# Kernel optimization log

Measured on AMD Instinct MI355X. Metric: run time of the kernel, lower is better.

The kernel has to match this reference:

```python
import math
import jax, jax.numpy as jnp
import numpy as np

B, H, W, C = 4, 64, 64, 96
SSM_RATIO = 2.0
D_INNER = int(SSM_RATIO * C)   # 192
D_STATE = 4
DT_RANK = math.ceil(C / 16)    # 6
K = 4                          # 4 scan directions
D_CONV = 3


def layer_norm(x, g, b, eps=1e-5):
    mu = jnp.mean(x, axis=-1, keepdims=True)
    var = jnp.var(x, axis=-1, keepdims=True)
    return (x - mu) / jnp.sqrt(var + eps) * g + b


def cross_scan(x):
    # x: (B, D, H, W) -> (B, K=4, D, L); dirs: row-major, col-major, and their reverses
    b, d, h, w = x.shape
    s0 = x.reshape(b, d, h * w)
    s1 = jnp.transpose(x, (0, 1, 3, 2)).reshape(b, d, h * w)
    return jnp.stack([s0, s1, s0[..., ::-1], s1[..., ::-1]], axis=1)


def cross_merge(ys, h, w):
    # ys: (B, K=4, D, L) -> (B, D, L); inverse of cross_scan, summed over directions
    b, k, d, L = ys.shape
    ys = ys[:, 0:2] + ys[:, 2:4][..., ::-1]
    y0 = ys[:, 0]
    y1 = jnp.transpose(ys[:, 1].reshape(b, d, w, h), (0, 1, 3, 2)).reshape(b, d, L)
    return y0 + y1


def selective_scan(u, dt, A, Bm, Cm, D4):
    # u, dt: (B,K,D,L); A: (K,D,N); Bm, Cm: (B,K,N,L); D4: (K,D)
    u_l = jnp.moveaxis(u, -1, 0)    # (L,B,K,D)
    dt_l = jnp.moveaxis(dt, -1, 0)
    B_l = jnp.moveaxis(Bm, -1, 0)   # (L,B,K,N)
    C_l = jnp.moveaxis(Cm, -1, 0)

    def step(h, inp):
        u_t, dt_t, B_t, C_t = inp
        dA = jnp.exp(dt_t[..., None] * A)                              # (B,K,D,N)
        h = h * dA + dt_t[..., None] * B_t[:, :, None, :] * u_t[..., None]
        y = jnp.sum(h * C_t[:, :, None, :], axis=-1)                   # (B,K,D)
        return h, y

    h0 = jnp.zeros(u.shape[:3] + (A.shape[-1],), u.dtype)
    _, ys = jax.lax.scan(step, h0, (u_l, dt_l, B_l, C_l))
    return jnp.moveaxis(ys, 0, -1) + D4[None, :, :, None] * u


def _block(x_rgb, x_e, in_proj_x_w, in_proj_e_w, conv_x_w, conv_x_b, conv_e_w, conv_e_b,
           x_proj_weight, dt_projs_weight, dt_projs_bias, A_logs, Ds,
           ln_r_g, ln_r_b, ln_e_g, ln_e_b, out_proj_x_w, out_proj_e_w):
    b, h, w, c = x_rgb.shape
    Din, N, R = D_INNER, D_STATE, DT_RANK

    xr = jnp.einsum('bhwc,dc->bhwd', x_rgb, in_proj_x_w)
    xe = jnp.einsum('bhwc,dc->bhwd', x_e, in_proj_e_w)
    xr = jnp.transpose(xr, (0, 3, 1, 2))  # (B,Din,H,W)
    xe = jnp.transpose(xe, (0, 3, 1, 2))

    def dwconv(x, wt, bias):
        y = jax.lax.conv_general_dilated(x, wt, (1, 1), 'SAME', feature_group_count=Din)
        return jax.nn.silu(y + bias[None, :, None, None])

    xr = dwconv(xr, conv_x_w, conv_x_b)
    xe = dwconv(xe, conv_e_w, conv_e_b)

    xs_r = cross_scan(xr)  # (B,K,Din,L)
    xs_e = cross_scan(xe)

    def proj(xs):
        dbl = jnp.einsum('bkdl,kcd->bkcl', xs, x_proj_weight)
        dtl, Bm, Cm = dbl[:, :, :R], dbl[:, :, R:R + N], dbl[:, :, R + N:]
        dtl = jnp.einsum('bkrl,kdr->bkdl', dtl, dt_projs_weight)
        dtl = jax.nn.softplus(dtl + dt_projs_bias[None, :, :, None])
        return dtl, Bm, Cm

    dt_r, B_r, C_r = proj(xs_r)
    dt_e, B_e, C_e = proj(xs_e)

    A = -jnp.exp(A_logs).reshape(K, Din, N)
    D4 = Ds.reshape(K, Din)

    # cross fusion: each modality's scan reads out through the OTHER modality's C
    y_r = selective_scan(xs_r, dt_r, A, B_r, C_e, D4)
    y_e = selective_scan(xs_e, dt_e, A, B_e, C_r, D4)

    y_r = cross_merge(y_r, h, w)  # (B,Din,L)
    y_e = cross_merge(y_e, h, w)

    y_r = layer_norm(jnp.transpose(y_r, (0, 2, 1)), ln_r_g, ln_r_b).reshape(b, h, w, Din)
    y_e = layer_norm(jnp.transpose(y_e, (0, 2, 1)), ln_e_g, ln_e_b).reshape(b, h, w, Din)

    out_r = jnp.einsum('bhwd,cd->bhwc', y_r, out_proj_x_w)
    out_e = jnp.einsum('bhwd,cd->bhwc', y_e, out_proj_e_w)

    # residual add of the wrapping block (drop_path=0, mlp_ratio=0)
    return x_rgb + out_r, x_e + out_e


def setup_inputs():
    key = jax.random.key(0)
    ks = jax.random.split(key, 16)
    N, R, Din = D_STATE, DT_RANK, D_INNER

    def rn(k, shape, s=0.02):
        return (jax.random.normal(k, shape) * s).astype(jnp.float32)

    # dt bias: inverse-softplus of dt ~ U[1e-3, 0.1]  (mamba-style init)
    dt = jnp.exp(jax.random.uniform(ks[10], (K, Din)) * (np.log(0.1) - np.log(1e-3)) + np.log(1e-3))
    dt_bias = dt + jnp.log(-jnp.expm1(-dt))

    return {
        'x_rgb': jax.random.normal(ks[0], (B, H, W, C), jnp.float32),
        'x_e': jax.random.normal(ks[1], (B, H, W, C), jnp.float32),
        'in_proj_x_w': rn(ks[2], (Din, C)),
        'in_proj_e_w': rn(ks[3], (Din, C)),
        'conv_x_w': rn(ks[4], (Din, 1, D_CONV, D_CONV), 0.1),
        'conv_x_b': jnp.zeros((Din,), jnp.float32),
        'conv_e_w': rn(ks[5], (Din, 1, D_CONV, D_CONV), 0.1),
        'conv_e_b': jnp.zeros((Din,), jnp.float32),
        'x_proj_weight': rn(ks[6], (K, R + 2 * N, Din)),
        'dt_projs_weight': rn(ks[7], (K, Din, R), R ** -0.5),
        'dt_projs_bias': dt_bias.astype(jnp.float32),
        'A_logs': jnp.log(jnp.tile(jnp.arange(1, N + 1, dtype=jnp.float32), (K * Din, 1))),
        'Ds': jnp.ones((K * Din,), jnp.float32),
        'ln_r_g': jnp.ones((Din,), jnp.float32),
        'ln_r_b': jnp.zeros((Din,), jnp.float32),
        'ln_e_g': jnp.ones((Din,), jnp.float32),
        'ln_e_b': jnp.zeros((Din,), jnp.float32),
        'out_proj_x_w': rn(ks[8], (C, Din)),
        'out_proj_e_w': rn(ks[9], (C, Din)),
    }


def reference(x_rgb, x_e, in_proj_x_w, in_proj_e_w, conv_x_w, conv_x_b, conv_e_w, conv_e_b,
              x_proj_weight, dt_projs_weight, dt_projs_bias, A_logs, Ds,
              ln_r_g, ln_r_b, ln_e_g, ln_e_b, out_proj_x_w, out_proj_e_w):
    return _block(x_rgb, x_e, in_proj_x_w, in_proj_e_w, conv_x_w, conv_x_b, conv_e_w, conv_e_b,
                  x_proj_weight, dt_projs_weight, dt_projs_bias, A_logs, Ds,
                  ln_r_g, ln_r_b, ln_e_g, ln_e_b, out_proj_x_w, out_proj_e_w)
```

## Files before the change

kernel.cpp:

```cpp
#include <hip/hip_runtime.h>

#define BB 4
#define HH 64
#define WW 64
#define CC 96
#define DIN 192
#define NS 4
#define RR 6
#define KK 4
#define LL 4096
#define NPOS (BB*LL)
#define NPD ((size_t)NPOS*DIN)
#define NDBC ((size_t)BB*KK*LL*14)
#define NCHUNK 128
#define CLEN 32
#define NCHAIN 32
#define PB 8

__device__ __forceinline__ int map_pos(int k, int l){
  switch(k){
    case 0: return l;
    case 1: { int wi=l>>6, hi=l&63; return hi*WW+wi; }
    case 2: return LL-1-l;
    default:{ int lr=LL-1-l; int wi=lr>>6, hi=lr&63; return hi*WW+wi; }
  }
}
__device__ __forceinline__ int pos_stride(int k){
  return (k==0) ? 1 : (k==1) ? WW : (k==2) ? -1 : -WW;
}

__global__ __launch_bounds__(DIN) void inproj_kernel(
    const float* __restrict__ x_rgb, const float* __restrict__ x_e,
    const float* __restrict__ w_r,   const float* __restrict__ w_e,
    float* __restrict__ xproj_r,    float* __restrict__ xproj_e){
  int blk = blockIdx.x;
  int m = blk / (NPOS/PB); int g = blk % (NPOS/PB);
  size_t rem0 = (size_t)g * PB;
  const float* x = m ? x_e : x_rgb;
  const float* w = m ? w_e : w_r;
  float* o = m ? xproj_e : xproj_r;
  __shared__ float xs[PB][CC];
  __shared__ float wt[DIN][17];
  int t = threadIdx.x;
  for(int idx=t; idx<PB*CC; idx+=DIN) xs[idx/CC][idx%CC] = x[rem0*CC + idx];
  float acc[PB];
  #pragma unroll
  for(int p=0;p<PB;p++) acc[p]=0.f;
  for(int c0=0; c0<CC; c0+=16){
    __syncthreads();
    for(int idx=t; idx<DIN*16; idx+=DIN){
      int dd = idx>>4, cc = idx&15;
      wt[dd][cc] = w[(size_t)dd*CC + c0 + cc];
    }
    __syncthreads();
    #pragma unroll
    for(int cc=0; cc<16; cc++){
      float wv = wt[t][cc];
      #pragma unroll
      for(int p=0;p<PB;p++) acc[p] += xs[p][c0+cc]*wv;
    }
  }
  #pragma unroll
  for(int p=0;p<PB;p++) o[(rem0+p)*DIN + t] = acc[p];
}

__global__ __launch_bounds__(DIN) void conv_kernel(
    const float* __restrict__ xproj_r, const float* __restrict__ xproj_e,
    const float* __restrict__ cw_r, const float* __restrict__ cb_r,
    const float* __restrict__ cw_e, const float* __restrict__ cb_e,
    float* __restrict__ xconv_r, float* __restrict__ xconv_e){
  int blk = blockIdx.x;
  int m = blk / NPOS; int rem = blk % NPOS;
  int b = rem / LL, p = rem % LL;
  int y = p >> 6, x = p & 63;
  const float* in = (m ? xproj_e : xproj_r) + (size_t)b*LL*DIN;
  const float* cw = m ? cw_e : cw_r;
  const float* cb = m ? cb_e : cb_r;
  float* out = m ? xconv_e : xconv_r;
  int d = threadIdx.x;
  float acc = cb[d];
  #pragma unroll
  for(int dy=-1;dy<=1;dy++){
    int yy = y+dy; if(yy<0 || yy>=HH) continue;
    #pragma unroll
    for(int dx=-1;dx<=1;dx++){
      int xx = x+dx; if(xx<0 || xx>=WW) continue;
      acc += in[(size_t)(yy*WW+xx)*DIN + d] * cw[d*9 + (dy+1)*3 + (dx+1)];
    }
  }
  float s = acc / (1.f + __expf(-acc));
  out[(size_t)(b*LL+p)*DIN + d] = s;
}

#define TPOS 32
__global__ __launch_bounds__(256) void projbc_kernel(
    const float* __restrict__ xconv_r, const float* __restrict__ xconv_e,
    const float* __restrict__ xpw,
    float* __restrict__ dtBC_r, float* __restrict__ dtBC_e){
  int blk = blockIdx.x;
  int m = blk / (BB*LL/TPOS); int rem = blk % (BB*LL/TPOS);
  int b = rem / (LL/TPOS); int p0 = (rem % (LL/TPOS)) * TPOS;
  const float* xc = (m ? xconv_e : xconv_r) + ((size_t)b*LL + p0)*DIN;
  float* o = (m ? dtBC_e : dtBC_r) + (size_t)b*KK*LL*14;

  __shared__ float xs[TPOS*97];
  __shared__ float wsd[56*97];

  int t = threadIdx.x;
  int g = t >> 5;
  int pl = t & 31;

  float acc[7];
  #pragma unroll
  for(int j=0;j<7;j++) acc[j]=0.f;

  for(int dt0=0; dt0<DIN; dt0+=96){
    __syncthreads();
    for(int idx=t; idx<TPOS*96; idx+=256){
      int r = idx/96, ccol = idx%96;
      xs[r*97+ccol] = xc[(size_t)r*DIN + dt0 + ccol];
    }
    for(int idx=t; idx<56*96; idx+=256){
      int r = idx/96, ccol = idx%96;
      wsd[r*97+ccol] = xpw[(size_t)r*DIN + dt0 + ccol];
    }
    __syncthreads();
    const float* xrow = &xs[pl*97];
    #pragma unroll 4
    for(int d=0; d<96; d++){
      float xv = xrow[d];
      #pragma unroll
      for(int j=0;j<7;j++) acc[j] += wsd[(g*7+j)*97 + d]*xv;
    }
  }

  int p = p0 + pl;
  int ptr_ = (p&63)*64 + (p>>6);
  #pragma unroll
  for(int j=0;j<7;j++){
    int cbar = g*7+j;
    int k = cbar/14, c = cbar%14;
    int l = (k==0) ? p : (k==1) ? ptr_ : (k==2) ? (LL-1-p) : (LL-1-ptr_);
    o[((size_t)k*LL + l)*14 + c] = acc[j];
  }
}

__global__ __launch_bounds__(DIN) void scan_p1_kernel(
    const float* __restrict__ xconv_r, const float* __restrict__ xconv_e,
    const float* __restrict__ dtBC_r, const float* __restrict__ dtBC_e,
    const float* __restrict__ dtw, const float* __restrict__ dtb,
    const float* __restrict__ A_logs,
    float* __restrict__ trans_S, float* __restrict__ sumdt){
  int ch = blockIdx.x / NCHUNK;
  int cidx = blockIdx.x % NCHUNK;
  int m = ch >> 4, b = (ch>>2)&3, k = ch&3;
  int d = threadIdx.x;
  int l0 = cidx*CLEN;

  float4 al = *(const float4*)&A_logs[(size_t)(k*DIN+d)*NS];
  float A0=-__expf(al.x), A1=-__expf(al.y), A2=-__expf(al.z), A3=-__expf(al.w);
  float Wd[RR];
  #pragma unroll
  for(int r=0;r<RR;r++) Wd[r] = dtw[((size_t)k*DIN + d)*RR + r];
  float bias = dtb[k*DIN+d];

  const float* xc    = (m ? xconv_e : xconv_r) + (size_t)b*LL*DIN;
  const float* dbc_m = (m ? dtBC_e : dtBC_r) + ((size_t)b*KK + k)*LL*14;

  __shared__ float4 db4[CLEN][4];
  __shared__ float u_s[CLEN*DIN];
  float* dbf = (float*)db4;

  for(int idx=d; idx<CLEN*14; idx+=DIN){
    int i = idx/14, j = idx%14;
    int slot = (j<6) ? (8+j) : (j-6);
    dbf[i*16+slot] = dbc_m[(size_t)l0*14 + idx];
  }
  int stride = pos_stride(k);
  int pos0 = map_pos(k, l0);
  #pragma unroll 8
  for(int i=0;i<CLEN;i++)
    u_s[i*DIN+d] = xc[(size_t)(pos0+i*stride)*DIN + d];
  __syncthreads();

  float h0=0.f,h1=0.f,h2=0.f,h3=0.f,sd=0.f;
  #pragma unroll 4
  for(int i=0;i<CLEN;i++){
    float4 Bv  = db4[i][0];
    float4 d03 = db4[i][2];
    float4 d45 = db4[i][3];
    float dtr = fmaf(d03.x,Wd[0], fmaf(d03.y,Wd[1], fmaf(d03.z,Wd[2],
                fmaf(d03.w,Wd[3], fmaf(d45.x,Wd[4], fmaf(d45.y,Wd[5], bias))))));
    float dt = fmaxf(dtr,0.f) + __logf(1.f + __expf(-fabsf(dtr)));
    sd += dt;
    float u = u_s[i*DIN + d];
    float dtu = dt*u;
    h0 = fmaf(h0, __expf(dt*A0), dtu*Bv.x);
    h1 = fmaf(h1, __expf(dt*A1), dtu*Bv.y);
    h2 = fmaf(h2, __expf(dt*A2), dtu*Bv.z);
    h3 = fmaf(h3, __expf(dt*A3), dtu*Bv.w);
  }
  size_t base = ((size_t)(ch*NCHUNK + cidx)*NS)*DIN + d;
  trans_S[base          ] = h0;
  trans_S[base +   DIN  ] = h1;
  trans_S[base + 2*DIN  ] = h2;
  trans_S[base + 3*DIN  ] = h3;
  sumdt[(size_t)(ch*NCHUNK + cidx)*DIN + d] = sd;
}

__global__ __launch_bounds__(DIN) void scan_p2_kernel(
    const float* __restrict__ trans_S, const float* __restrict__ sumdt,
    const float* __restrict__ A_logs, float* __restrict__ hin){
  int ch = blockIdx.x; int k = ch & 3; int d = threadIdx.x;
  float4 al = *(const float4*)&A_logs[(size_t)(k*DIN+d)*NS];
  float A[NS] = {-__expf(al.x), -__expf(al.y), -__expf(al.z), -__expf(al.w)};
  float h[NS] = {0.f,0.f,0.f,0.f};
  for(int c0=0;c0<NCHUNK;c0+=4){
    float S[4][NS], sdv[4];
    #pragma unroll
    for(int cc=0;cc<4;cc++){
      size_t base = ((size_t)(ch*NCHUNK + c0+cc)*NS)*DIN + d;
      #pragma unroll
      for(int n=0;n<NS;n++) S[cc][n] = trans_S[base + (size_t)n*DIN];
      sdv[cc] = sumdt[(size_t)(ch*NCHUNK + c0+cc)*DIN + d];
    }
    #pragma unroll
    for(int cc=0;cc<4;cc++){
      size_t base = ((size_t)(ch*NCHUNK + c0+cc)*NS)*DIN + d;
      #pragma unroll
      for(int n=0;n<NS;n++) hin[base + (size_t)n*DIN] = h[n];
      #pragma unroll
      for(int n=0;n<NS;n++) h[n] = fmaf(h[n], __expf(A[n]*sdv[cc]), S[cc][n]);
    }
  }
}

__global__ __launch_bounds__(DIN) void scan_p3_kernel(
    const float* __restrict__ xconv_r, const float* __restrict__ xconv_e,
    const float* __restrict__ dtBC_r, const float* __restrict__ dtBC_e,
    const float* __restrict__ dtw, const float* __restrict__ dtb,
    const float* __restrict__ A_logs, const float* __restrict__ Ds,
    const float* __restrict__ hin,
    float* __restrict__ ym_r, float* __restrict__ ym_e){
  int ch = blockIdx.x / NCHUNK;
  int cidx = blockIdx.x % NCHUNK;
  int m = ch >> 4, b = (ch>>2)&3, k = ch&3;
  int d = threadIdx.x;
  int l0 = cidx*CLEN;

  float4 al = *(const float4*)&A_logs[(size_t)(k*DIN+d)*NS];
  float A0=-__expf(al.x), A1=-__expf(al.y), A2=-__expf(al.z), A3=-__expf(al.w);
  float Wd[RR];
  #pragma unroll
  for(int r=0;r<RR;r++) Wd[r] = dtw[((size_t)k*DIN + d)*RR + r];
  float bias = dtb[k*DIN+d];
  float Dv = Ds[k*DIN+d];

  const float* xc    = (m ? xconv_e : xconv_r) + (size_t)b*LL*DIN;
  const float* dbc_m = (m ? dtBC_e : dtBC_r) + ((size_t)b*KK + k)*LL*14;
  const float* dbc_o = (m ? dtBC_r : dtBC_e) + ((size_t)b*KK + k)*LL*14;
  float* ym = (m ? ym_e : ym_r) + (size_t)b*LL*DIN;

  __shared__ float4 db4[CLEN][4];
  __shared__ float u_s[CLEN*DIN];
  float* dbf = (float*)db4;

  for(int idx=d; idx<CLEN*14; idx+=DIN){
    int i = idx/14, j = idx%14;
    int slot = (j<6) ? (8+j) : (j-6);
    dbf[i*16+slot] = dbc_m[(size_t)l0*14 + idx];
  }
  for(int idx=d; idx<CLEN*NS; idx+=DIN){
    int i = idx>>2, j = idx&3;
    dbf[i*16 + 4 + j] = dbc_o[(size_t)(l0+i)*14 + 10 + j];
  }
  int stride = pos_stride(k);
  int pos0 = map_pos(k, l0);
  #pragma unroll 8
  for(int i=0;i<CLEN;i++)
    u_s[i*DIN+d] = xc[(size_t)(pos0+i*stride)*DIN + d];
  __syncthreads();

  size_t hbase = ((size_t)(ch*NCHUNK + cidx)*NS)*DIN + d;
  float h0=hin[hbase], h1=hin[hbase+DIN], h2=hin[hbase+2*DIN], h3=hin[hbase+3*DIN];

  #pragma unroll 4
  for(int i=0;i<CLEN;i++){
    float4 Bv  = db4[i][0];
    float4 Cv  = db4[i][1];
    float4 d03 = db4[i][2];
    float4 d45 = db4[i][3];
    float dtr = fmaf(d03.x,Wd[0], fmaf(d03.y,Wd[1], fmaf(d03.z,Wd[2],
                fmaf(d03.w,Wd[3], fmaf(d45.x,Wd[4], fmaf(d45.y,Wd[5], bias))))));
    float dt = fmaxf(dtr,0.f) + __logf(1.f + __expf(-fabsf(dtr)));
    float u = u_s[i*DIN + d];
    float dtu = dt*u;
    h0 = fmaf(h0, __expf(dt*A0), dtu*Bv.x);
    h1 = fmaf(h1, __expf(dt*A1), dtu*Bv.y);
    h2 = fmaf(h2, __expf(dt*A2), dtu*Bv.z);
    h3 = fmaf(h3, __expf(dt*A3), dtu*Bv.w);
    float y = fmaf(h0,Cv.x, fmaf(h1,Cv.y, fmaf(h2,Cv.z, fmaf(h3,Cv.w, Dv*u))));
    atomicAdd(&ym[(size_t)(pos0+i*stride)*DIN + d], y);
  }
}

__global__ __launch_bounds__(DIN) void ln_out_kernel(
    const float* __restrict__ ym_r, const float* __restrict__ ym_e,
    const float* __restrict__ ln_rg, const float* __restrict__ ln_rb,
    const float* __restrict__ ln_eg, const float* __restrict__ ln_eb,
    const float* __restrict__ opw_r, const float* __restrict__ opw_e,
    const float* __restrict__ x_rgb, const float* __restrict__ x_e,
    float* __restrict__ out){
  int blk = blockIdx.x;
  int m = blk / (NPOS/PB); int g = blk % (NPOS/PB);
  size_t rem0 = (size_t)g * PB;
  const float* ym = (m ? ym_e : ym_r) + rem0*DIN;
  int t = threadIdx.x;
  int wid = t>>6;

  float v[PB];
  #pragma unroll
  for(int p=0;p<PB;p++) v[p] = ym[(size_t)p*DIN + t];

  __shared__ float red_s[PB][3], red_q[PB][3];
  #pragma unroll
  for(int p=0;p<PB;p++){
    float s = v[p], q = v[p]*v[p];
    #pragma unroll
    for(int off=32; off>0; off>>=1){ s += __shfl_down(s,off); q += __shfl_down(q,off); }
    if((t&63)==0){ red_s[p][wid]=s; red_q[p][wid]=q; }
  }
  __syncthreads();

  const float* gg = m ? ln_eg : ln_rg;
  const float* be = m ? ln_eb : ln_rb;
  __shared__ float yn_s[PB][DIN];
  float gv = gg[t], bv = be[t];
  #pragma unroll
  for(int p=0;p<PB;p++){
    float S = red_s[p][0]+red_s[p][1]+red_s[p][2];
    float Q = red_q[p][0]+red_q[p][1]+red_q[p][2];
    float mu  = S*(1.f/DIN);
    float var = Q*(1.f/DIN) - mu*mu;
    float inv = rsqrtf(var + 1e-5f);
    yn_s[p][t] = (v[p]-mu)*inv*gv + bv;
  }
  __syncthreads();

  int c = t % CC;
  int pbase = t / CC;
  const float* w = (m ? opw_e : opw_r) + (size_t)c*DIN;
  float acc[4] = {0.f,0.f,0.f,0.f};
  for(int dd=0; dd<DIN; dd++){
    float wv = w[dd];
    #pragma unroll
    for(int pp=0;pp<4;pp++) acc[pp] += yn_s[pbase + 2*pp][dd]*wv;
  }
  const float* xin = m ? x_e : x_rgb;
  #pragma unroll
  for(int pp=0;pp<4;pp++){
    size_t rem = rem0 + pbase + 2*pp;
    size_t oi = (size_t)m*NPOS*CC + rem*CC + c;
    out[oi] = acc[pp] + xin[rem*CC + c];
  }
}

extern "C" void kernel_launch(void* const* d_in, const int* in_sizes, int n_in,
                              void* d_out, int out_size, void* d_ws, size_t ws_size,
                              hipStream_t stream){
  const float* x_rgb = (const float*)d_in[0];
  const float* x_e   = (const float*)d_in[1];
  const float* ipw_r = (const float*)d_in[2];
  const float* ipw_e = (const float*)d_in[3];
  const float* cw_r  = (const float*)d_in[4];
  const float* cb_r  = (const float*)d_in[5];
  const float* cw_e  = (const float*)d_in[6];
  const float* cb_e  = (const float*)d_in[7];
  const float* xpw   = (const float*)d_in[8];
  const float* dtw   = (const float*)d_in[9];
  const float* dtb   = (const float*)d_in[10];
  const float* Alog  = (const float*)d_in[11];
  const float* Ds_   = (const float*)d_in[12];
  const float* ln_rg = (const float*)d_in[13];
  const float* ln_rb = (const float*)d_in[14];
  const float* ln_eg = (const float*)d_in[15];
  const float* ln_eb = (const float*)d_in[16];
  const float* opw_r = (const float*)d_in[17];
  const float* opw_e = (const float*)d_in[18];
  float* out = (float*)d_out;

  float* ws = (float*)d_ws;
  float* xproj_r = ws;
  float* xproj_e = ws + NPD;
  float* xconv_r = ws + 2*NPD;
  float* xconv_e = ws + 3*NPD;
  float* dtBC_r  = ws + 4*NPD;
  float* dtBC_e  = ws + 4*NPD + NDBC;
  float* trans_S = ws + 4*NPD + 2*NDBC;
  float* sumdt   = trans_S + (size_t)NCHAIN*NCHUNK*NS*DIN;
  float* hin     = sumdt   + (size_t)NCHAIN*NCHUNK*DIN;
  float* ym_r = xproj_r;
  float* ym_e = xproj_e;

  inproj_kernel<<<2*NPOS/PB, DIN, 0, stream>>>(x_rgb, x_e, ipw_r, ipw_e, xproj_r, xproj_e);
  conv_kernel<<<2*NPOS, DIN, 0, stream>>>(xproj_r, xproj_e, cw_r, cb_r, cw_e, cb_e, xconv_r, xconv_e);
  projbc_kernel<<<2*BB*(LL/TPOS), 256, 0, stream>>>(xconv_r, xconv_e, xpw, dtBC_r, dtBC_e);
  scan_p1_kernel<<<NCHAIN*NCHUNK, DIN, 0, stream>>>(xconv_r, xconv_e, dtBC_r, dtBC_e,
                                                    dtw, dtb, Alog, trans_S, sumdt);
  scan_p2_kernel<<<NCHAIN, DIN, 0, stream>>>(trans_S, sumdt, Alog, hin);
  hipMemsetAsync(ym_r, 0, 2*NPD*sizeof(float), stream);
  scan_p3_kernel<<<NCHAIN*NCHUNK, DIN, 0, stream>>>(xconv_r, xconv_e, dtBC_r, dtBC_e,
                                                    dtw, dtb, Alog, Ds_, hin, ym_r, ym_e);
  ln_out_kernel<<<2*NPOS/PB, DIN, 0, stream>>>(ym_r, ym_e, ln_rg, ln_rb, ln_eg, ln_eb,
                                               opw_r, opw_e, x_rgb, x_e, out);
}
```

Before: 463.3 us.

## Pair forward and reverse scan directions per block, drop atomics and memset

Each scan_p3 block now handles a forward direction chunk and the matching chunk of its reversed direction, which touch the same spatial positions. The block loads the shared u tile once, writes the first result with a plain store and read-modify-writes the second. Row and column directions go to two separate output buffers that the LN kernel sums, so the float atomics and the output memset are no longer needed. The cost is two extra full-size workspace buffers, an extra read in the LN kernel, and twice the serial work per block with half as many blocks.

```diff
diff --git a/kernel.cpp b/kernel.cpp
--- a/kernel.cpp
+++ b/kernel.cpp
@@ -241,71 +241,118 @@
     const float* __restrict__ dtw, const float* __restrict__ dtb,
     const float* __restrict__ A_logs, const float* __restrict__ Ds,
     const float* __restrict__ hin,
-    float* __restrict__ ym_r, float* __restrict__ ym_e){
-  int ch = blockIdx.x / NCHUNK;
-  int cidx = blockIdx.x % NCHUNK;
-  int m = ch >> 4, b = (ch>>2)&3, k = ch&3;
+    float* __restrict__ ym_a_r, float* __restrict__ ym_a_e,
+    float* __restrict__ ym_b_r, float* __restrict__ ym_b_e){
+  int blk = blockIdx.x;
+  int cidx = blk % NCHUNK;
+  int rem  = blk / NCHUNK;
+  int pg = rem & 1; rem >>= 1;
+  int b  = rem & 3; int m = rem >> 2;
+  int kA = pg, kB = pg + 2;
+  int cidx2 = NCHUNK-1-cidx;
+  int l0A = cidx*CLEN, l0B = cidx2*CLEN;
+
   int d = threadIdx.x;
-  int l0 = cidx*CLEN;
-
-  float4 al = *(const float4*)&A_logs[(size_t)(k*DIN+d)*NS];
-  float A0=-__expf(al.x), A1=-__expf(al.y), A2=-__expf(al.z), A3=-__expf(al.w);
-  float Wd[RR];
-  #pragma unroll
-  for(int r=0;r<RR;r++) Wd[r] = dtw[((size_t)k*DIN + d)*RR + r];
-  float bias = dtb[k*DIN+d];
-  float Dv = Ds[k*DIN+d];
-
-  const float* xc    = (m ? xconv_e : xconv_r) + (size_t)b*LL*DIN;
-  const float* dbc_m = (m ? dtBC_e : dtBC_r) + ((size_t)b*KK + k)*LL*14;
-  const float* dbc_o = (m ? dtBC_r : dtBC_e) + ((size_t)b*KK + k)*LL*14;
-  float* ym = (m ? ym_e : ym_r) + (size_t)b*LL*DIN;
-
-  __shared__ float4 db4[CLEN][4];
+  int st = pos_stride(kA);
+  int pos0 = map_pos(kA, l0A);
+
+  const float* xc = (m ? xconv_e : xconv_r) + (size_t)b*LL*DIN;
+  const float* dbc_own = (m ? dtBC_e : dtBC_r) + (size_t)b*KK*LL*14;
+  const float* dbc_oth = (m ? dtBC_r : dtBC_e) + (size_t)b*KK*LL*14;
+  float* ym = (pg==0) ? (m ? ym_a_e : ym_a_r) : (m ? ym_b_e : ym_b_r);
+  ym += (size_t)b*LL*DIN;
+
+  __shared__ float4 db4A[CLEN][4];
+  __shared__ float4 db4B[CLEN][4];
   __shared__ float u_s[CLEN*DIN];
-  float* dbf = (float*)db4;
+  float* dbfA = (float*)db4A;
+  float* dbfB = (float*)db4B;
 
   for(int idx=d; idx<CLEN*14; idx+=DIN){
     int i = idx/14, j = idx%14;
     int slot = (j<6) ? (8+j) : (j-6);
-    dbf[i*16+slot] = dbc_m[(size_t)l0*14 + idx];
+    dbfA[i*16+slot] = dbc_own[((size_t)kA*LL + l0A)*14 + idx];
+    dbfB[i*16+slot] = dbc_own[((size_t)kB*LL + l0B)*14 + idx];
   }
   for(int idx=d; idx<CLEN*NS; idx+=DIN){
     int i = idx>>2, j = idx&3;
-    dbf[i*16 + 4 + j] = dbc_o[(size_t)(l0+i)*14 + 10 + j];
-  }
-  int stride = pos_stride(k);
-  int pos0 = map_pos(k, l0);
+    dbfA[i*16 + 4 + j] = dbc_oth[((size_t)kA*LL + l0A + i)*14 + 10 + j];
+    dbfB[i*16 + 4 + j] = dbc_oth[((size_t)kB*LL + l0B + i)*14 + 10 + j];
+  }
   #pragma unroll 8
   for(int i=0;i<CLEN;i++)
-    u_s[i*DIN+d] = xc[(size_t)(pos0+i*stride)*DIN + d];
+    u_s[i*DIN+d] = xc[(size_t)(pos0+i*st)*DIN + d];
   __syncthreads();
 
-  size_t hbase = ((size_t)(ch*NCHUNK + cidx)*NS)*DIN + d;
-  float h0=hin[hbase], h1=hin[hbase+DIN], h2=hin[hbase+2*DIN], h3=hin[hbase+3*DIN];
-
-  #pragma unroll 4
-  for(int i=0;i<CLEN;i++){
-    float4 Bv  = db4[i][0];
-    float4 Cv  = db4[i][1];
-    float4 d03 = db4[i][2];
-    float4 d45 = db4[i][3];
-    float dtr = fmaf(d03.x,Wd[0], fmaf(d03.y,Wd[1], fmaf(d03.z,Wd[2],
-                fmaf(d03.w,Wd[3], fmaf(d45.x,Wd[4], fmaf(d45.y,Wd[5], bias))))));
-    float dt = fmaxf(dtr,0.f) + __logf(1.f + __expf(-fabsf(dtr)));
-    float u = u_s[i*DIN + d];
-    float dtu = dt*u;
-    h0 = fmaf(h0, __expf(dt*A0), dtu*Bv.x);
-    h1 = fmaf(h1, __expf(dt*A1), dtu*Bv.y);
-    h2 = fmaf(h2, __expf(dt*A2), dtu*Bv.z);
-    h3 = fmaf(h3, __expf(dt*A3), dtu*Bv.w);
-    float y = fmaf(h0,Cv.x, fmaf(h1,Cv.y, fmaf(h2,Cv.z, fmaf(h3,Cv.w, Dv*u))));
-    atomicAdd(&ym[(size_t)(pos0+i*stride)*DIN + d], y);
+  {
+    int k = kA;
+    float4 al = *(const float4*)&A_logs[(size_t)(k*DIN+d)*NS];
+    float A0=-__expf(al.x), A1=-__expf(al.y), A2=-__expf(al.z), A3=-__expf(al.w);
+    float Wd[RR];
+    #pragma unroll
+    for(int r=0;r<RR;r++) Wd[r] = dtw[((size_t)k*DIN + d)*RR + r];
+    float bias = dtb[k*DIN+d];
+    float Dv = Ds[k*DIN+d];
+    int chA = (m*4+b)*4 + kA;
+    size_t hbase = ((size_t)(chA*NCHUNK + cidx)*NS)*DIN + d;
+    float h0=hin[hbase], h1=hin[hbase+DIN], h2=hin[hbase+2*DIN], h3=hin[hbase+3*DIN];
+    #pragma unroll 4
+    for(int i=0;i<CLEN;i++){
+      float4 Bv  = db4A[i][0];
+      float4 Cv  = db4A[i][1];
+      float4 d03 = db4A[i][2];
+      float4 d45 = db4A[i][3];
+      float dtr = fmaf(d03.x,Wd[0], fmaf(d03.y,Wd[1], fmaf(d03.z,Wd[2],
+                  fmaf(d03.w,Wd[3], fmaf(d45.x,Wd[4], fmaf(d45.y,Wd[5], bias))))));
+      float dt = fmaxf(dtr,0.f) + __logf(1.f + __expf(-fabsf(dtr)));
+      float u = u_s[i*DIN + d];
+      float dtu = dt*u;
+      h0 = fmaf(h0, __expf(dt*A0), dtu*Bv.x);
+      h1 = fmaf(h1, __expf(dt*A1), dtu*Bv.y);
+      h2 = fmaf(h2, __expf(dt*A2), dtu*Bv.z);
+      h3 = fmaf(h3, __expf(dt*A3), dtu*Bv.w);
+      float y = fmaf(h0,Cv.x, fmaf(h1,Cv.y, fmaf(h2,Cv.z, fmaf(h3,Cv.w, Dv*u))));
+      ym[(size_t)(pos0+i*st)*DIN + d] = y;
+    }
+  }
+  {
+    int k = kB;
+    float4 al = *(const float4*)&A_logs[(size_t)(k*DIN+d)*NS];
+    float A0=-__expf(al.x), A1=-__expf(al.y), A2=-__expf(al.z), A3=-__expf(al.w);
+    float Wd[RR];
+    #pragma unroll
+    for(int r=0;r<RR;r++) Wd[r] = dtw[((size_t)k*DIN + d)*RR + r];
+    float bias = dtb[k*DIN+d];
+    float Dv = Ds[k*DIN+d];
+    int chB = (m*4+b)*4 + kB;
+    size_t hbase = ((size_t)(chB*NCHUNK + cidx2)*NS)*DIN + d;
+    float h0=hin[hbase], h1=hin[hbase+DIN], h2=hin[hbase+2*DIN], h3=hin[hbase+3*DIN];
+    #pragma unroll 4
+    for(int j=0;j<CLEN;j++){
+      int pi = CLEN-1-j;
+      float4 Bv  = db4B[j][0];
+      float4 Cv  = db4B[j][1];
+      float4 d03 = db4B[j][2];
+      float4 d45 = db4B[j][3];
+      float dtr = fmaf(d03.x,Wd[0], fmaf(d03.y,Wd[1], fmaf(d03.z,Wd[2],
+                  fmaf(d03.w,Wd[3], fmaf(d45.x,Wd[4], fmaf(d45.y,Wd[5], bias))))));
+      float dt = fmaxf(dtr,0.f) + __logf(1.f + __expf(-fabsf(dtr)));
+      float u = u_s[pi*DIN + d];
+      float dtu = dt*u;
+      h0 = fmaf(h0, __expf(dt*A0), dtu*Bv.x);
+      h1 = fmaf(h1, __expf(dt*A1), dtu*Bv.y);
+      h2 = fmaf(h2, __expf(dt*A2), dtu*Bv.z);
+      h3 = fmaf(h3, __expf(dt*A3), dtu*Bv.w);
+      float y = fmaf(h0,Cv.x, fmaf(h1,Cv.y, fmaf(h2,Cv.z, fmaf(h3,Cv.w, Dv*u))));
+      size_t a = (size_t)(pos0+pi*st)*DIN + d;
+      ym[a] += y;
+    }
   }
 }
 
 __global__ __launch_bounds__(DIN) void ln_out_kernel(
-    const float* __restrict__ ym_r, const float* __restrict__ ym_e,
+    const float* __restrict__ ym_a_r, const float* __restrict__ ym_a_e,
+    const float* __restrict__ ym_b_r, const float* __restrict__ ym_b_e,
     const float* __restrict__ ln_rg, const float* __restrict__ ln_rb,
     const float* __restrict__ ln_eg, const float* __restrict__ ln_eb,
     const float* __restrict__ opw_r, const float* __restrict__ opw_e,
@@ -314,13 +361,14 @@
   int blk = blockIdx.x;
   int m = blk / (NPOS/PB); int g = blk % (NPOS/PB);
   size_t rem0 = (size_t)g * PB;
-  const float* ym = (m ? ym_e : ym_r) + rem0*DIN;
+  const float* yma = (m ? ym_a_e : ym_a_r) + rem0*DIN;
+  const float* ymb = (m ? ym_b_e : ym_b_r) + rem0*DIN;
   int t = threadIdx.x;
   int wid = t>>6;
 
   float v[PB];
   #pragma unroll
-  for(int p=0;p<PB;p++) v[p] = ym[(size_t)p*DIN + t];
+  for(int p=0;p<PB;p++) v[p] = yma[(size_t)p*DIN + t] + ymb[(size_t)p*DIN + t];
 
   __shared__ float red_s[PB][3], red_q[PB][3];
   #pragma unroll
@@ -399,8 +447,10 @@
   float* trans_S = ws + 4*NPD + 2*NDBC;
   float* sumdt   = trans_S + (size_t)NCHAIN*NCHUNK*NS*DIN;
   float* hin     = sumdt   + (size_t)NCHAIN*NCHUNK*DIN;
-  float* ym_r = xproj_r;
-  float* ym_e = xproj_e;
+  float* ym_b_r  = hin     + (size_t)NCHAIN*NCHUNK*NS*DIN;
+  float* ym_b_e  = ym_b_r + NPD;
+  float* ym_a_r = xproj_r;
+  float* ym_a_e = xproj_e;
 
   inproj_kernel<<<2*NPOS/PB, DIN, 0, stream>>>(x_rgb, x_e, ipw_r, ipw_e, xproj_r, xproj_e);
   conv_kernel<<<2*NPOS, DIN, 0, stream>>>(xproj_r, xproj_e, cw_r, cb_r, cw_e, cb_e, xconv_r, xconv_e);
@@ -408,9 +458,10 @@
   scan_p1_kernel<<<NCHAIN*NCHUNK, DIN, 0, stream>>>(xconv_r, xconv_e, dtBC_r, dtBC_e,
                                                     dtw, dtb, Alog, trans_S, sumdt);
   scan_p2_kernel<<<NCHAIN, DIN, 0, stream>>>(trans_S, sumdt, Alog, hin);
-  hipMemsetAsync(ym_r, 0, 2*NPD*sizeof(float), stream);
-  scan_p3_kernel<<<NCHAIN*NCHUNK, DIN, 0, stream>>>(xconv_r, xconv_e, dtBC_r, dtBC_e,
-                                                    dtw, dtb, Alog, Ds_, hin, ym_r, ym_e);
-  ln_out_kernel<<<2*NPOS/PB, DIN, 0, stream>>>(ym_r, ym_e, ln_rg, ln_rb, ln_eg, ln_eb,
+  scan_p3_kernel<<<2*BB*2*NCHUNK, DIN, 0, stream>>>(xconv_r, xconv_e, dtBC_r, dtBC_e,
+                                                    dtw, dtb, Alog, Ds_, hin,
+                                                    ym_a_r, ym_a_e, ym_b_r, ym_b_e);
+  ln_out_kernel<<<2*NPOS/PB, DIN, 0, stream>>>(ym_a_r, ym_a_e, ym_b_r, ym_b_e,
+                                               ln_rg, ln_rb, ln_eg, ln_eb,
                                                opw_r, opw_e, x_rgb, x_e, out);
 }
```

Result: faster. 420.4 us (-9.3%).
